# Kernel optimization log

Hardware: AMD Instinct MI355X
Metric: run time of the kernel (lower is better)

Reference implementation:

```python
import jax, jax.numpy as jnp
import numpy as np

N = 50000
E = 1600000
F_IN = 503
F_H = 128
NEG_SLOPE = 0.2


def setup_inputs() -> dict:
    key = jax.random.key(0)
    ks = jax.random.split(key, 24)
    s = 0.05
    inp = {
        "x": jax.random.normal(ks[0], (N, F_IN), jnp.float32),
        "edge_index": jax.random.randint(ks[1], (2, E), 0, N, jnp.int64),
        "edge_attr": jax.random.uniform(ks[2], (E, 1), jnp.float32),
        "input_mask": jax.random.uniform(ks[3], (N, 1), jnp.float32),
        # GATConv layer 1 (in=503, out=128, heads=1, edge_dim=1)
        "W1": jax.random.normal(ks[4], (F_IN, F_H), jnp.float32) * s,
        "b1": jnp.zeros((F_H,), jnp.float32),
        "as1": jax.random.normal(ks[5], (F_H,), jnp.float32) * s,
        "ad1": jax.random.normal(ks[6], (F_H,), jnp.float32) * s,
        "We1": jax.random.normal(ks[7], (1, F_H), jnp.float32) * s,
        "ae1": jax.random.normal(ks[8], (F_H,), jnp.float32) * s,
        # GATConv layer 2 (in=128, out=128)
        "W2": jax.random.normal(ks[9], (F_H, F_H), jnp.float32) * s,
        "b2": jnp.zeros((F_H,), jnp.float32),
        "as2": jax.random.normal(ks[10], (F_H,), jnp.float32) * s,
        "ad2": jax.random.normal(ks[11], (F_H,), jnp.float32) * s,
        "We2": jax.random.normal(ks[12], (1, F_H), jnp.float32) * s,
        "ae2": jax.random.normal(ks[13], (F_H,), jnp.float32) * s,
        # edge/node heads
        "Wb": jax.random.normal(ks[14], (F_H, 1), jnp.float32) * s,
        "bb": jnp.zeros((1,), jnp.float32),
        "Ww": jax.random.normal(ks[15], (F_H, 1), jnp.float32) * s,
        "bw": jnp.zeros((1,), jnp.float32),
    }
    return inp


def _gat_conv(x, src, dst, ea, W, b, a_src_vec, a_dst_vec, We, a_edge_vec):
    """PyG GATConv, heads=1, add_self_loops=True, fill_value='mean'."""
    n = x.shape[0]
    loop = jnp.arange(n)
    # self-loop edge attrs = mean of incoming edge attrs (0 if none)
    deg = jax.ops.segment_sum(jnp.ones(dst.shape, ea.dtype), dst, num_segments=n)
    ea_loop = jax.ops.segment_sum(ea, dst, num_segments=n) / jnp.maximum(deg, 1.0)[:, None]
    s = jnp.concatenate([src, loop])
    d = jnp.concatenate([dst, loop])
    ea2 = jnp.concatenate([ea, ea_loop], axis=0)  # [E+N, 1]

    h = x @ W                              # [N, F_H]
    a_s = h @ a_src_vec                    # [N]
    a_d = h @ a_dst_vec                    # [N]
    a_e = (ea2 @ We) @ a_edge_vec          # [E+N]

    alpha = jax.nn.leaky_relu(a_s[s] + a_d[d] + a_e, NEG_SLOPE)
    # scatter-softmax over destination neighborhoods (every node has a self loop)
    m = jax.lax.stop_gradient(jax.ops.segment_max(alpha, d, num_segments=n))
    ex = jnp.exp(alpha - m[d])
    den = jax.ops.segment_sum(ex, d, num_segments=n)
    coef = ex / den[d]                     # [E+N]

    out = jax.ops.segment_sum(coef[:, None] * h[s], d, num_segments=n)
    return out + b


def reference(x, edge_index, edge_attr, input_mask,
              W1, b1, as1, ad1, We1, ae1,
              W2, b2, as2, ad2, We2, ae2,
              Wb, bb, Ww, bw):
    src, dst = edge_index[0], edge_index[1]
    h = jax.nn.relu(_gat_conv(x, src, dst, edge_attr, W1, b1, as1, ad1, We1, ae1))
    h = jax.nn.relu(_gat_conv(h, src, dst, edge_attr, W2, b2, as2, ad2, We2, ae2))
    b_out = (h @ Wb + bb) * input_mask          # [N, 1]
    # directed graph: is_directed() is True, so use all edges
    w = ((h[src] + h[dst]) * 0.5) @ Ww + bw     # [E, 1]
    return (w, b_out)
```

## Files before the change

kernel.cpp:

```cpp
#include <hip/hip_runtime.h>
#include <hip/hip_fp16.h>

#define FH 128
#define NEG_SLOPE 0.2f
#define GBM 64
#define GBK 64
#define HT 1024
#define TB 8
#define NWMAX 12512

typedef _Float16 f16x8 __attribute__((ext_vector_type(8)));
typedef float f32x4 __attribute__((ext_vector_type(4)));

__global__ __launch_bounds__(HT) void hist_kernel(const int* __restrict__ ei,
                                                  unsigned short* __restrict__ hist,
                                                  int E, int N) {
  __shared__ unsigned int lh[NWMAX];
  const int b = blockIdx.x, tid = threadIdx.x;
  const int nw = (N + 3) >> 2;
  for (int j = tid; j < nw; j += HT) lh[j] = 0u;
  __syncthreads();
  const int i0 = b * (HT * TB) + tid * TB;
  if (i0 + TB <= E) {
    int4 da = *(const int4*)&ei[E + i0];
    int4 db = *(const int4*)&ei[E + i0 + 4];
    int dv[8] = {da.x, da.y, da.z, da.w, db.x, db.y, db.z, db.w};
    #pragma unroll
    for (int k = 0; k < 8; k++)
      atomicAdd(&lh[dv[k] >> 2], 1u << ((dv[k] & 3) * 8));
  } else {
    for (int i = i0; i < E; i++) {
      int d = ei[E + i];
      atomicAdd(&lh[d >> 2], 1u << ((d & 3) * 8));
    }
  }
  __syncthreads();
  unsigned short* hb = hist + (size_t)b * N;
  for (int j = tid; j < nw; j += HT) {
    unsigned v = lh[j];
    int bin = j * 4;
    if (bin + 3 < N) {
      ushort4 o;
      o.x = v & 255u; o.y = (v >> 8) & 255u; o.z = (v >> 16) & 255u; o.w = v >> 24;
      *(ushort4*)&hb[bin] = o;
    } else {
      for (int k = 0; k < 4 && bin + k < N; k++) hb[bin + k] = (v >> (k * 8)) & 255u;
    }
  }
}

__global__ void colscan_kernel(unsigned short* __restrict__ hist,
                               int* __restrict__ cnt, int N, int NBr) {
  int bin = blockIdx.x * 256 + threadIdx.x;
  if (bin >= N) return;
  int s = 0;
  for (int b = 0; b < NBr; b++) {
    int t = hist[(size_t)b * N + bin];
    hist[(size_t)b * N + bin] = (unsigned short)s;
    s += t;
  }
  cnt[bin] = s;
}

__global__ void scan_blocksum(const int* __restrict__ deg, int* __restrict__ bsum, int n) {
  __shared__ int sm[256];
  int i = blockIdx.x * 256 + threadIdx.x;
  sm[threadIdx.x] = (i < n) ? deg[i] : 0;
  __syncthreads();
  for (int off = 128; off > 0; off >>= 1) {
    if (threadIdx.x < off) sm[threadIdx.x] += sm[threadIdx.x + off];
    __syncthreads();
  }
  if (threadIdx.x == 0) bsum[blockIdx.x] = sm[0];
}

__global__ void scan_bsum(int* __restrict__ bsum, int nb, int* __restrict__ rowptr, int N) {
  __shared__ int sm[1024];
  int t = threadIdx.x;
  int v = (t < nb) ? bsum[t] : 0;
  sm[t] = v;
  __syncthreads();
  for (int off = 1; off < 1024; off <<= 1) {
    int u = (t >= off) ? sm[t - off] : 0;
    __syncthreads();
    sm[t] += u;
    __syncthreads();
  }
  if (t < nb) bsum[t] = sm[t] - v;
  if (t == 1023) rowptr[N] = sm[1023];
}

__global__ void scan_final(const int* __restrict__ deg, const int* __restrict__ bsum,
                           int* __restrict__ rowptr, int n) {
  __shared__ int sm[256];
  int i = blockIdx.x * 256 + threadIdx.x;
  int v = (i < n) ? deg[i] : 0;
  sm[threadIdx.x] = v;
  __syncthreads();
  for (int off = 1; off < 256; off <<= 1) {
    int u = (threadIdx.x >= off) ? sm[threadIdx.x - off] : 0;
    __syncthreads();
    sm[threadIdx.x] += u;
    __syncthreads();
  }
  if (i < n) rowptr[i] = bsum[blockIdx.x] + sm[threadIdx.x] - v;
}

__global__ __launch_bounds__(HT) void place_kernel(const int* __restrict__ ei,
                                                   const float* __restrict__ ea,
                                                   const int* __restrict__ rowptr,
                                                   const unsigned short* __restrict__ off,
                                                   unsigned int* __restrict__ pack,
                                                   int E, int N) {
  __shared__ unsigned int lc[NWMAX];
  const int b = blockIdx.x, tid = threadIdx.x;
  const int nw = (N + 3) >> 2;
  for (int j = tid; j < nw; j += HT) lc[j] = 0u;
  __syncthreads();
  const unsigned short* __restrict__ ob = off + (size_t)b * N;
  const int i0 = b * (HT * TB) + tid * TB;
  if (i0 + TB <= E) {
    int4 sa = *(const int4*)&ei[i0];
    int4 sb = *(const int4*)&ei[i0 + 4];
    int4 da = *(const int4*)&ei[E + i0];
    int4 db = *(const int4*)&ei[E + i0 + 4];
    float4 aa = *(const float4*)&ea[i0];
    float4 ab = *(const float4*)&ea[i0 + 4];
    int sv[8] = {sa.x, sa.y, sa.z, sa.w, sb.x, sb.y, sb.z, sb.w};
    int dv[8] = {da.x, da.y, da.z, da.w, db.x, db.y, db.z, db.w};
    float av[8] = {aa.x, aa.y, aa.z, aa.w, ab.x, ab.y, ab.z, ab.w};
    unsigned rr[8];
    #pragma unroll
    for (int k = 0; k < 8; k++)
      rr[k] = atomicAdd(&lc[dv[k] >> 2], 1u << ((dv[k] & 3) * 8));
    int pos[8];
    #pragma unroll
    for (int k = 0; k < 8; k++)
      pos[k] = rowptr[dv[k]] + (int)ob[dv[k]] + (int)((rr[k] >> ((dv[k] & 3) * 8)) & 255u);
    #pragma unroll
    for (int k = 0; k < 8; k++)
      pack[pos[k]] = ((unsigned)sv[k] << 16) | __half_as_ushort(__float2half(av[k]));
  } else {
    for (int i = i0; i < E; i++) {
      int d = ei[E + i];
      unsigned r = atomicAdd(&lc[d >> 2], 1u << ((d & 3) * 8));
      int local = (r >> ((d & 3) * 8)) & 255;
      int pos = rowptr[d] + (int)ob[d] + local;
      pack[pos] = ((unsigned)ei[i] << 16) | __half_as_ushort(__float2half(ea[i]));
    }
  }
}

__global__ void cvec_kernel(const float* __restrict__ We1, const float* __restrict__ ae1,
                            const float* __restrict__ We2, const float* __restrict__ ae2,
                            float* __restrict__ cv) {
  int l = threadIdx.x;
  float s1 = We1[l] * ae1[l] + We1[l + 64] * ae1[l + 64];
  float s2 = We2[l] * ae2[l] + We2[l + 64] * ae2[l + 64];
  for (int off = 32; off; off >>= 1) { s1 += __shfl_down(s1, off); s2 += __shfl_down(s2, off); }
  if (l == 0) { cv[0] = s1; cv[1] = s2; }
}

__global__ void wcvt_kernel(const float* __restrict__ W, __half* __restrict__ Wt,
                            int K, int Kpad) {
  int idx = blockIdx.x * 256 + threadIdx.x;
  if (idx >= 128 * Kpad) return;
  int n = idx / Kpad, k = idx - n * Kpad;
  Wt[idx] = (k < K) ? __float2half(W[(size_t)k * 128 + n]) : __float2half(0.f);
}

__global__ __launch_bounds__(256, 4) void mfma_gemm_kernel(
    const float* __restrict__ X, const __half* __restrict__ Wt_,
    const float* __restrict__ avs, const float* __restrict__ avd,
    __half* __restrict__ H16, float* __restrict__ a_s, float* __restrict__ a_d,
    int M, int K, int Kpad) {
  __shared__ _Float16 Bl[2 * 8 * 64 * 8];
  const _Float16* __restrict__ Wt = (const _Float16*)Wt_;
  const int tid  = threadIdx.x;
  const int lane = tid & 63;
  const int w    = tid >> 6;
  const int m0   = blockIdx.x * GBM;

  f32x4 acc[8];
  #pragma unroll
  for (int i = 0; i < 8; i++) acc[i] = (f32x4){0.f, 0.f, 0.f, 0.f};

  const int arow   = m0 + w * 16 + (lane & 15);
  const int arow_c = arow < M ? arow : (M - 1);
  const float* __restrict__ Xrow = X + (size_t)arow_c * K;
  const int kgrp = (lane >> 4) * 8;

  const int sg = tid & 7, snb = tid >> 3;

  for (int k0 = 0; k0 < Kpad; k0 += GBK) {
    #pragma unroll
    for (int i = 0; i < 4; i++) {
      int n = snb + 32 * i;
      f16x8 v = *(const f16x8*)(Wt + (size_t)n * Kpad + k0 + sg * 8);
      int kt = sg >> 2, nt = n >> 4;
      int fl = (n & 15) + (sg & 3) * 16;
      *(f16x8*)&Bl[((kt * 8 + nt) * 64 + fl) * 8] = v;
    }
    __syncthreads();
    const bool fast = (k0 + GBK <= K);
    #pragma unroll
    for (int kt = 0; kt < 2; kt++) {
      int kb = k0 + kt * 32 + kgrp;
      f16x8 af;
      if (fast) {
        #pragma unroll
        for (int j = 0; j < 8; j++) af[j] = (_Float16)Xrow[kb + j];
      } else {
        #pragma unroll
        for (int j = 0; j < 8; j++)
          af[j] = (kb + j < K) ? (_Float16)Xrow[kb + j] : (_Float16)0.f;
      }
      #pragma unroll
      for (int nt = 0; nt < 8; nt++) {
        f16x8 bf = *(const f16x8*)&Bl[((kt * 8 + nt) * 64 + lane) * 8];
        acc[nt] = __builtin_amdgcn_mfma_f32_16x16x32_f16(af, bf, acc[nt], 0, 0, 0);
      }
    }
    __syncthreads();
  }

  const int rbase = m0 + w * 16 + (lane >> 4) * 4;
  const int col   = lane & 15;
  float as_v[8], ad_v[8];
  #pragma unroll
  for (int nt = 0; nt < 8; nt++) {
    as_v[nt] = avs[nt * 16 + col];
    ad_v[nt] = avd[nt * 16 + col];
  }
  #pragma unroll
  for (int r = 0; r < 4; r++) {
    int gm = rbase + r;
    float ps = 0.f, pd = 0.f;
    #pragma unroll
    for (int nt = 0; nt < 8; nt++) {
      ps += acc[nt][r] * as_v[nt];
      pd += acc[nt][r] * ad_v[nt];
    }
    #pragma unroll
    for (int msk = 1; msk < 16; msk <<= 1) {
      ps += __shfl_xor(ps, msk);
      pd += __shfl_xor(pd, msk);
    }
    if (gm < M) {
      #pragma unroll
      for (int nt = 0; nt < 8; nt++)
        H16[(size_t)gm * FH + nt * 16 + col] = __float2half(acc[nt][r]);
      if (col == 0) { a_s[gm] = ps; a_d[gm] = pd; }
    }
  }
}

__global__ __launch_bounds__(256) void agg_kernel(
    const __half* __restrict__ H16, const int* __restrict__ rowptr,
    const unsigned int* __restrict__ pack,
    const float* __restrict__ a_s, const float* __restrict__ a_d,
    const float* __restrict__ cv, int cidx,
    const float* __restrict__ bias,
    float* __restrict__ Hout, int N) {
  const int node = (blockIdx.x * 256 + threadIdx.x) >> 6;
  const int lane = threadIdx.x & 63;
  const int slot = lane >> 4, sl = lane & 15;
  if (node >= N) return;
  const _Float16* __restrict__ Hh = (const _Float16*)H16;
  const float c   = cv[cidx];
  const float adn = a_d[node];
  const int beg = rowptr[node], end = rowptr[node + 1];

  float acc[8] = {0.f, 0.f, 0.f, 0.f, 0.f, 0.f, 0.f, 0.f};
  float den = 0.f, ea_tot = 0.f;

  for (int p = beg + slot; p < end; p += 4) {
    unsigned w0 = pack[p];
    int s0 = w0 >> 16;
    float e0 = __half2float(__ushort_as_half((unsigned short)(w0 & 0xffff)));
    float al = a_s[s0] + adn + c * e0;
    al = fmaxf(al, NEG_SLOPE * al);
    float ex = __expf(al);
    f16x8 h = *(const f16x8*)(Hh + (size_t)s0 * FH + sl * 8);
    ea_tot += e0;
    den += ex;
    #pragma unroll
    for (int j = 0; j < 8; j++) acc[j] += ex * (float)h[j];
  }
  ea_tot += __shfl_xor(ea_tot, 16); ea_tot += __shfl_xor(ea_tot, 32);
  den    += __shfl_xor(den,    16); den    += __shfl_xor(den,    32);
  #pragma unroll
  for (int j = 0; j < 8; j++) {
    acc[j] += __shfl_xor(acc[j], 16);
    acc[j] += __shfl_xor(acc[j], 32);
  }
  {
    int dg = end - beg;
    float eal = ea_tot / fmaxf((float)dg, 1.f);
    float al = a_s[node] + adn + c * eal;
    al = fmaxf(al, NEG_SLOPE * al);
    float ex = __expf(al);
    f16x8 h = *(const f16x8*)(Hh + (size_t)node * FH + sl * 8);
    den += ex;
    #pragma unroll
    for (int j = 0; j < 8; j++) acc[j] += ex * (float)h[j];
  }
  if (slot == 0) {
    float inv = 1.f / den;
    float4 b0 = *(const float4*)&bias[sl * 8];
    float4 b1 = *(const float4*)&bias[sl * 8 + 4];
    float4 o0, o1;
    o0.x = fmaxf(acc[0] * inv + b0.x, 0.f);
    o0.y = fmaxf(acc[1] * inv + b0.y, 0.f);
    o0.z = fmaxf(acc[2] * inv + b0.z, 0.f);
    o0.w = fmaxf(acc[3] * inv + b0.w, 0.f);
    o1.x = fmaxf(acc[4] * inv + b1.x, 0.f);
    o1.y = fmaxf(acc[5] * inv + b1.y, 0.f);
    o1.z = fmaxf(acc[6] * inv + b1.z, 0.f);
    o1.w = fmaxf(acc[7] * inv + b1.w, 0.f);
    *(float4*)&Hout[(size_t)node * FH + sl * 8]     = o0;
    *(float4*)&Hout[(size_t)node * FH + sl * 8 + 4] = o1;
  }
}

__global__ void node_head_kernel(const float* __restrict__ H, const float* __restrict__ Wb,
                                 const float* __restrict__ bb, const float* __restrict__ Ww,
                                 const float* __restrict__ mask,
                                 float* __restrict__ bout, float* __restrict__ p, int N) {
  int gid = blockIdx.x * 256 + threadIdx.x;
  int node = gid >> 6, lane = threadIdx.x & 63;
  if (node >= N) return;
  float2 h  = *(const float2*)&H[(size_t)node * FH + lane * 2];
  float2 wb = *(const float2*)&Wb[lane * 2];
  float2 ww = *(const float2*)&Ww[lane * 2];
  float sb = h.x * wb.x + h.y * wb.y;
  float sw = h.x * ww.x + h.y * ww.y;
  for (int off = 32; off; off >>= 1) { sb += __shfl_down(sb, off); sw += __shfl_down(sw, off); }
  if (lane == 0) {
    bout[node] = (sb + bb[0]) * mask[node];
    p[node]    = sw;
  }
}

__global__ void edge_head_kernel(const int* __restrict__ ei, const float* __restrict__ p,
                                 const float* __restrict__ bw, float* __restrict__ w, int E) {
  int base = (blockIdx.x * 256 + threadIdx.x) * 4;
  if (base >= E) return;
  float b = bw[0];
  if (base + 4 <= E) {
    int4 s = *(const int4*)&ei[base];
    int4 d = *(const int4*)&ei[E + base];
    float4 o;
    o.x = 0.5f * (p[s.x] + p[d.x]) + b;
    o.y = 0.5f * (p[s.y] + p[d.y]) + b;
    o.z = 0.5f * (p[s.z] + p[d.z]) + b;
    o.w = 0.5f * (p[s.w] + p[d.w]) + b;
    *(float4*)&w[base] = o;
  } else {
    for (int e = base; e < E; e++)
      w[e] = 0.5f * (p[ei[e]] + p[ei[E + e]]) + b;
  }
}

extern "C" void kernel_launch(void* const* d_in, const int* in_sizes, int n_in,
                              void* d_out, int out_size, void* d_ws, size_t ws_size,
                              hipStream_t stream) {
  (void)n_in; (void)out_size; (void)ws_size;
  const float* x    = (const float*)d_in[0];
  const int*   ei   = (const int*)  d_in[1];
  const float* ea   = (const float*)d_in[2];
  const float* mask = (const float*)d_in[3];
  const float* W1   = (const float*)d_in[4];
  const float* b1   = (const float*)d_in[5];
  const float* as1  = (const float*)d_in[6];
  const float* ad1  = (const float*)d_in[7];
  const float* We1  = (const float*)d_in[8];
  const float* ae1  = (const float*)d_in[9];
  const float* W2   = (const float*)d_in[10];
  const float* b2   = (const float*)d_in[11];
  const float* as2  = (const float*)d_in[12];
  const float* ad2  = (const float*)d_in[13];
  const float* We2  = (const float*)d_in[14];
  const float* ae2  = (const float*)d_in[15];
  const float* Wb   = (const float*)d_in[16];
  const float* bb   = (const float*)d_in[17];
  const float* Ww   = (const float*)d_in[18];
  const float* bw   = (const float*)d_in[19];

  const int N  = in_sizes[3];
  const int E  = in_sizes[1] / 2;
  const int K1 = in_sizes[0] / N;
  const int K1p = (K1 + GBK - 1) & ~(GBK - 1);
  const int NBr = (E + HT * TB - 1) / (HT * TB);

  char* ws = (char*)d_ws;
  size_t off0 = 0;
  auto alloc = [&](size_t bytes) -> char* {
    char* q = ws + off0;
    off0 = (off0 + bytes + 255) & ~(size_t)255;
    return q;
  };
  int*   cnt    = (int*)  alloc((size_t)N * 4);
  int*   rowptr = (int*)  alloc((size_t)(N + 1) * 4);
  int*   bsum   = (int*)  alloc(1024 * 4);
  unsigned short* hist = (unsigned short*)alloc((size_t)NBr * N * 2);
  unsigned int*   pack = (unsigned int*)  alloc((size_t)E * 4);
  float* a_s    = (float*)alloc((size_t)N * 4);
  float* a_d    = (float*)alloc((size_t)N * 4);
  __half* H16   = (__half*)alloc((size_t)N * FH * 2);
  float* HB     = (float*)alloc((size_t)N * FH * 4);
  float* pbuf   = (float*)alloc((size_t)N * 4);
  float* cv     = (float*)alloc(8);
  __half* W1t   = (__half*)alloc((size_t)FH * K1p * 2);
  __half* W2t   = (__half*)alloc((size_t)FH * FH * 2);

  float* w_out = (float*)d_out;
  float* b_out = (float*)d_out + E;

  const int nb  = (N + 255) / 256;
  const int gb  = (N + GBM - 1) / GBM;
  const int wbk = ((size_t)N * 64 + 255) / 256;
  const int ab  = (N + 3) / 4;
  const int eb4 = (E + 1023) / 1024;

  hist_kernel   <<<NBr, HT, 0, stream>>>(ei, hist, E, N);
  colscan_kernel<<<nb, 256, 0, stream>>>(hist, cnt, N, NBr);
  scan_blocksum <<<nb, 256, 0, stream>>>(cnt, bsum, N);
  scan_bsum     <<<1, 1024, 0, stream>>>(bsum, nb, rowptr, N);
  scan_final    <<<nb, 256, 0, stream>>>(cnt, bsum, rowptr, N);
  place_kernel  <<<NBr, HT, 0, stream>>>(ei, ea, rowptr, hist, pack, E, N);
  cvec_kernel   <<<1, 64, 0, stream>>>(We1, ae1, We2, ae2, cv);
  wcvt_kernel   <<<(128 * K1p + 255) / 256, 256, 0, stream>>>(W1, W1t, K1, K1p);
  wcvt_kernel   <<<(128 * FH + 255) / 256, 256, 0, stream>>>(W2, W2t, FH, FH);

  mfma_gemm_kernel<<<gb, 256, 0, stream>>>(x, W1t, as1, ad1, H16, a_s, a_d, N, K1, K1p);
  agg_kernel  <<<ab, 256, 0, stream>>>(H16, rowptr, pack, a_s, a_d, cv, 0, b1, HB, N);
  mfma_gemm_kernel<<<gb, 256, 0, stream>>>(HB, W2t, as2, ad2, H16, a_s, a_d, N, FH, FH);
  agg_kernel  <<<ab, 256, 0, stream>>>(H16, rowptr, pack, a_s, a_d, cv, 1, b2, HB, N);
  node_head_kernel<<<wbk, 256, 0, stream>>>(HB, Wb, bb, Ww, mask, b_out, pbuf, N);
  edge_head_kernel<<<eb4, 256, 0, stream>>>(ei, pbuf, bw, w_out, E);
}
```

Baseline: 310.7 us.

## Permute hidden feature layout for vector H16 stores and prefetch GEMM A-tile

The GEMM epilogue now writes each row's eight fp16 outputs as one 16-byte store instead of eight scattered 2-byte stores. This stores features in a permuted order, and the permutation is absorbed downstream: W2's K dimension, the bias load in the aggregation kernel, and the node-head weight indexing. The GEMM also register-prefetches the next K-tile of X while computing the current one, and loads the B tile into LDS with a linear write pattern. The cost is extra registers for the prefetch buffer and strided bias/weight reads in the consumers.

After: 340.7 us. 1.1x slower.

```diff
diff --git a/kernel.cpp b/kernel.cpp
--- a/kernel.cpp
+++ b/kernel.cpp
@@ -8,6 +8,7 @@
 #define HT 1024
 #define TB 8
 #define NWMAX 12512
+
 
 typedef _Float16 f16x8 __attribute__((ext_vector_type(8)));
 typedef float f32x4 __attribute__((ext_vector_type(4)));
@@ -162,10 +163,11 @@
 }
 
 __global__ void wcvt_kernel(const float* __restrict__ W, __half* __restrict__ Wt,
-                            int K, int Kpad) {
+                            int K, int Kpad, int perm) {
   int idx = blockIdx.x * 256 + threadIdx.x;
   if (idx >= 128 * Kpad) return;
-  int n = idx / Kpad, k = idx - n * Kpad;
+  int n = idx / Kpad, p = idx - n * Kpad;
+  int k = perm ? ((p & 7) * 16 + (p >> 3)) : p;
   Wt[idx] = (k < K) ? __float2half(W[(size_t)k * 128 + n]) : __float2half(0.f);
 }
 
@@ -190,31 +192,51 @@
   const float* __restrict__ Xrow = X + (size_t)arow_c * K;
   const int kgrp = (lane >> 4) * 8;
 
-  const int sg = tid & 7, snb = tid >> 3;
+  float rn[2][8];
+  {
+    const bool fast = (GBK <= K);
+    #pragma unroll
+    for (int kt = 0; kt < 2; kt++) {
+      int kb = kt * 32 + kgrp;
+      #pragma unroll
+      for (int j = 0; j < 8; j++)
+        rn[kt][j] = (fast || kb + j < K) ? Xrow[kb + j] : 0.f;
+    }
+  }
 
   for (int k0 = 0; k0 < Kpad; k0 += GBK) {
     #pragma unroll
     for (int i = 0; i < 4; i++) {
-      int n = snb + 32 * i;
+      int s = tid + 256 * i;
+      int kt = s >> 9, rem = s & 511;
+      int nt = rem >> 6, fl = rem & 63;
+      int n  = nt * 16 + (fl & 15);
+      int sg = kt * 4 + (fl >> 4);
       f16x8 v = *(const f16x8*)(Wt + (size_t)n * Kpad + k0 + sg * 8);
-      int kt = sg >> 2, nt = n >> 4;
-      int fl = (n & 15) + (sg & 3) * 16;
-      *(f16x8*)&Bl[((kt * 8 + nt) * 64 + fl) * 8] = v;
-    }
-    __syncthreads();
-    const bool fast = (k0 + GBK <= K);
-    #pragma unroll
-    for (int kt = 0; kt < 2; kt++) {
-      int kb = k0 + kt * 32 + kgrp;
-      f16x8 af;
-      if (fast) {
-        #pragma unroll
-        for (int j = 0; j < 8; j++) af[j] = (_Float16)Xrow[kb + j];
-      } else {
+      *(f16x8*)&Bl[s * 8] = v;
+    }
+    __syncthreads();
+    float rv[2][8];
+    #pragma unroll
+    for (int kt = 0; kt < 2; kt++)
+      #pragma unroll
+      for (int j = 0; j < 8; j++) rv[kt][j] = rn[kt][j];
+    int k0n = k0 + GBK;
+    if (k0n < Kpad) {
+      const bool fastn = (k0n + GBK <= K);
+      #pragma unroll
+      for (int kt = 0; kt < 2; kt++) {
+        int kb = k0n + kt * 32 + kgrp;
         #pragma unroll
         for (int j = 0; j < 8; j++)
-          af[j] = (kb + j < K) ? (_Float16)Xrow[kb + j] : (_Float16)0.f;
+          rn[kt][j] = (fastn || kb + j < K) ? Xrow[kb + j] : 0.f;
       }
+    }
+    #pragma unroll
+    for (int kt = 0; kt < 2; kt++) {
+      f16x8 af;
+      #pragma unroll
+      for (int j = 0; j < 8; j++) af[j] = (_Float16)rv[kt][j];
       #pragma unroll
       for (int nt = 0; nt < 8; nt++) {
         f16x8 bf = *(const f16x8*)&Bl[((kt * 8 + nt) * 64 + lane) * 8];
@@ -247,9 +269,14 @@
       pd += __shfl_xor(pd, msk);
     }
     if (gm < M) {
-      #pragma unroll
-      for (int nt = 0; nt < 8; nt++)
-        H16[(size_t)gm * FH + nt * 16 + col] = __float2half(acc[nt][r]);
+      __half2 h0 = __floats2half2_rn(acc[0][r], acc[1][r]);
+      __half2 h1 = __floats2half2_rn(acc[2][r], acc[3][r]);
+      __half2 h2 = __floats2half2_rn(acc[4][r], acc[5][r]);
+      __half2 h3 = __floats2half2_rn(acc[6][r], acc[7][r]);
+      uint4 u;
+      u.x = *(unsigned*)&h0; u.y = *(unsigned*)&h1;
+      u.z = *(unsigned*)&h2; u.w = *(unsigned*)&h3;
+      *(uint4*)&H16[(size_t)gm * FH + col * 8] = u;
       if (col == 0) { a_s[gm] = ps; a_d[gm] = pd; }
     }
   }
@@ -307,17 +334,18 @@
   }
   if (slot == 0) {
     float inv = 1.f / den;
-    float4 b0 = *(const float4*)&bias[sl * 8];
-    float4 b1 = *(const float4*)&bias[sl * 8 + 4];
+    float bi[8];
+    #pragma unroll
+    for (int j = 0; j < 8; j++) bi[j] = bias[j * 16 + sl];
     float4 o0, o1;
-    o0.x = fmaxf(acc[0] * inv + b0.x, 0.f);
-    o0.y = fmaxf(acc[1] * inv + b0.y, 0.f);
-    o0.z = fmaxf(acc[2] * inv + b0.z, 0.f);
-    o0.w = fmaxf(acc[3] * inv + b0.w, 0.f);
-    o1.x = fmaxf(acc[4] * inv + b1.x, 0.f);
-    o1.y = fmaxf(acc[5] * inv + b1.y, 0.f);
-    o1.z = fmaxf(acc[6] * inv + b1.z, 0.f);
-    o1.w = fmaxf(acc[7] * inv + b1.w, 0.f);
+    o0.x = fmaxf(acc[0] * inv + bi[0], 0.f);
+    o0.y = fmaxf(acc[1] * inv + bi[1], 0.f);
+    o0.z = fmaxf(acc[2] * inv + bi[2], 0.f);
+    o0.w = fmaxf(acc[3] * inv + bi[3], 0.f);
+    o1.x = fmaxf(acc[4] * inv + bi[4], 0.f);
+    o1.y = fmaxf(acc[5] * inv + bi[5], 0.f);
+    o1.z = fmaxf(acc[6] * inv + bi[6], 0.f);
+    o1.w = fmaxf(acc[7] * inv + bi[7], 0.f);
     *(float4*)&Hout[(size_t)node * FH + sl * 8]     = o0;
     *(float4*)&Hout[(size_t)node * FH + sl * 8 + 4] = o1;
   }
@@ -330,11 +358,12 @@
   int gid = blockIdx.x * 256 + threadIdx.x;
   int node = gid >> 6, lane = threadIdx.x & 63;
   if (node >= N) return;
-  float2 h  = *(const float2*)&H[(size_t)node * FH + lane * 2];
-  float2 wb = *(const float2*)&Wb[lane * 2];
-  float2 ww = *(const float2*)&Ww[lane * 2];
-  float sb = h.x * wb.x + h.y * wb.y;
-  float sw = h.x * ww.x + h.y * ww.y;
+  int p0 = lane * 2, p1 = p0 + 1;
+  int f0 = ((p0 & 7) << 4) + (p0 >> 3);
+  int f1 = ((p1 & 7) << 4) + (p1 >> 3);
+  float2 h = *(const float2*)&H[(size_t)node * FH + p0];
+  float sb = h.x * Wb[f0] + h.y * Wb[f1];
+  float sw = h.x * Ww[f0] + h.y * Ww[f1];
   for (int off = 32; off; off >>= 1) { sb += __shfl_down(sb, off); sw += __shfl_down(sw, off); }
   if (lane == 0) {
     bout[node] = (sb + bb[0]) * mask[node];
@@ -430,8 +459,8 @@
   scan_final    <<<nb, 256, 0, stream>>>(cnt, bsum, rowptr, N);
   place_kernel  <<<NBr, HT, 0, stream>>>(ei, ea, rowptr, hist, pack, E, N);
   cvec_kernel   <<<1, 64, 0, stream>>>(We1, ae1, We2, ae2, cv);
-  wcvt_kernel   <<<(128 * K1p + 255) / 256, 256, 0, stream>>>(W1, W1t, K1, K1p);
-  wcvt_kernel   <<<(128 * FH + 255) / 256, 256, 0, stream>>>(W2, W2t, FH, FH);
+  wcvt_kernel   <<<(128 * K1p + 255) / 256, 256, 0, stream>>>(W1, W1t, K1, K1p, 0);
+  wcvt_kernel   <<<(128 * FH + 255) / 256, 256, 0, stream>>>(W2, W2t, FH, FH, 1);
 
   mfma_gemm_kernel<<<gb, 256, 0, stream>>>(x, W1t, as1, ad1, H16, a_s, a_d, N, K1, K1p);
   agg_kernel  <<<ab, 256, 0, stream>>>(H16, rowptr, pack, a_s, a_d, cv, 0, b1, HB, N);
```
